# Optimization experiments

Measured on AMD Instinct MI355X. Metric: run time of the kernel, lower is better.

## Reference

```python
import jax, jax.numpy as jnp
import numpy as np

FEAT = 36          # 4 + node_embedding_dim(32)
N_NODES = 24       # max_num_nodes_per_route
N_ROUTES = 48      # max_num_route
CUST_H = 128
CUST_OUT = 32
RNN_H = 128        # route_output_dim
B = 512


def _xavier(key, shape):
    fan_in, fan_out = shape[0], shape[1]
    lim = float(np.sqrt(6.0 / (fan_in + fan_out)))
    return jax.random.uniform(key, shape, jnp.float32, -lim, lim)


def setup_inputs() -> dict:
    key = jax.random.key(0)
    ks = jax.random.split(key, 24)
    inp = {
        "candidates": jax.random.normal(ks[0], (B, 2 * FEAT), jnp.float32),
        "customers": jax.random.normal(ks[1], (B, N_ROUTES, N_NODES * FEAT), jnp.float32),
        # Customer_Model MLP: 36 -> 128 (tanh) -> 32 (tanh)
        "cust_w1": _xavier(ks[2], (FEAT, CUST_H)),
        "cust_b1": jnp.zeros((CUST_H,), jnp.float32),
        "cust_w2": _xavier(ks[3], (CUST_H, CUST_OUT)),
        "cust_b2": jnp.zeros((CUST_OUT,), jnp.float32),
        # GRU layer 0 (input 32 -> hidden 128), gates order (r,z,n)
        "gru_wih0": _xavier(ks[4], (CUST_OUT, 3 * RNN_H)),
        "gru_whh0": _xavier(ks[5], (RNN_H, 3 * RNN_H)),
        "gru_bih0": jnp.zeros((3 * RNN_H,), jnp.float32),
        "gru_bhh0": jnp.zeros((3 * RNN_H,), jnp.float32),
        # GRU layer 1 (128 -> 128)
        "gru_wih1": _xavier(ks[6], (RNN_H, 3 * RNN_H)),
        "gru_whh1": _xavier(ks[7], (RNN_H, 3 * RNN_H)),
        "gru_bih1": jnp.zeros((3 * RNN_H,), jnp.float32),
        "gru_bhh1": jnp.zeros((3 * RNN_H,), jnp.float32),
        # candidate head and final MLP
        "cand_w": _xavier(ks[8], (2 * FEAT, 64)),
        "cand_b": jnp.zeros((64,), jnp.float32),
        "fc1_w": _xavier(ks[9], (RNN_H + 64, 128)),
        "fc1_b": jnp.zeros((128,), jnp.float32),
        "fc2_w": _xavier(ks[10], (128, 128)),
        "fc2_b": jnp.zeros((128,), jnp.float32),
        "fc3_w": _xavier(ks[11], (128, 1)),
        "fc3_b": jnp.zeros((1,), jnp.float32),
    }
    return inp


def _gru_layer(x_seq, wih, whh, bih, bhh):
    # x_seq: [T, N, in_dim]; returns [T, N, RNN_H]
    gi = jnp.einsum('tni,ih->tnh', x_seq, wih) + bih  # precompute input gates

    def step(h, gi_t):
        gh = h @ whh + bhh
        i_r, i_z, i_n = jnp.split(gi_t, 3, axis=-1)
        h_r, h_z, h_n = jnp.split(gh, 3, axis=-1)
        r = jax.nn.sigmoid(i_r + h_r)
        z = jax.nn.sigmoid(i_z + h_z)
        n = jnp.tanh(i_n + r * h_n)
        h_new = (1.0 - z) * n + z * h
        return h_new, h_new

    h0 = jnp.zeros((x_seq.shape[1], RNN_H), x_seq.dtype)
    _, out = jax.lax.scan(step, h0, gi)
    return out


def reference(candidates, customers, cust_w1, cust_b1, cust_w2, cust_b2,
              gru_wih0, gru_whh0, gru_bih0, gru_bhh0,
              gru_wih1, gru_whh1, gru_bih1, gru_bhh1,
              cand_w, cand_b, fc1_w, fc1_b, fc2_w, fc2_b, fc3_w, fc3_b):
    b = candidates.shape[0]
    x_c = candidates @ cand_w + cand_b                      # [B, 64]

    # all routes processed at once: fold routes into batch dim
    x = customers.reshape(b * N_ROUTES, N_NODES, FEAT)
    x = jnp.transpose(x, (1, 0, 2))                          # [T=24, B*48, 36]
    # Customer_Model MLP (tanh hidden, tanh output)
    x = jnp.tanh(jnp.tanh(x @ cust_w1 + cust_b1) @ cust_w2 + cust_b2)  # [24, B*48, 32]

    out = _gru_layer(x, gru_wih0, gru_whh0, gru_bih0, gru_bhh0)
    out = _gru_layer(out, gru_wih1, gru_whh1, gru_bih1, gru_bhh1)
    last = out[-1].reshape(b, N_ROUTES, RNN_H)               # last timestep per route
    x_r = last.mean(axis=1)                                  # mean over 48 routes
    # dropout is identity at inference

    h = jnp.concatenate([x_r, x_c], axis=1)                  # [B, 192]
    h = jnp.tanh(h @ fc1_w + fc1_b)
    h = jnp.tanh(h @ fc2_w + fc2_b)
    return h @ fc3_w + fc3_b                                 # [B, 1]
```

## Files before the change

### kernel.cpp

```cpp
#include <hip/hip_runtime.h>
#include <stdint.h>


#define NSEQ   24576
#define TSTEPS 24
#define SEQB   32

typedef __attribute__((ext_vector_type(8))) short bf16x8;
typedef __attribute__((ext_vector_type(4))) float floatx4;

#define PK_W1    0
#define PK_W2    8192
#define PK_WIH0  12288
#define PK_WHH0  24576
#define PK_WIH1  73728
#define PK_WHH1  122880
#define PK_END   172032
#define X2_EL    172032
#define HOUT_BYTE 38092800

#define MFMA(a,b,c) c = __builtin_amdgcn_mfma_f32_16x16x32_bf16(a, b, c, 0, 0, 0)

__device__ __forceinline__ uint16_t f2bf(float f) {
  uint32_t u = __float_as_uint(f);
  u += 0x7FFFu + ((u >> 16) & 1u);
  return (uint16_t)(u >> 16);
}
__device__ __forceinline__ uint32_t cvt_pk(float a, float b) {
  uint32_t r;
  asm("v_cvt_pk_bf16_f32 %0, %1, %2" : "=v"(r) : "v"(a), "v"(b));
  return r;
}
__device__ __forceinline__ float fast_sigmoid(float x) {
  float e = __builtin_amdgcn_exp2f(-1.4426950408889634f * x);
  return __builtin_amdgcn_rcpf(1.0f + e);
}
__device__ __forceinline__ float fast_tanh(float x) {
  float e = __builtin_amdgcn_exp2f(-2.8853900817779268f * x);
  return 2.0f * __builtin_amdgcn_rcpf(1.0f + e) - 1.0f;
}
__device__ __forceinline__ bf16x8 ldf(const uint16_t* p) {
  return *(const bf16x8*)p;
}

__global__ __launch_bounds__(256) void pack_weights(
    const float* __restrict__ w1, const float* __restrict__ w2,
    const float* __restrict__ wih0, const float* __restrict__ whh0,
    const float* __restrict__ wih1, const float* __restrict__ whh1,
    uint16_t* __restrict__ ws) {
  int idx = blockIdx.x * 256 + threadIdx.x;
  if (idx >= PK_END) return;
  const float* W; int N, KB, Kreal, base;
  if      (idx <  8192) { W = w1;   N = 128; KB = 2; Kreal = 36;  base = 0; }
  else if (idx < 12288) { W = w2;   N = 32;  KB = 4; Kreal = 128; base = 8192; }
  else if (idx < 24576) { W = wih0; N = 384; KB = 1; Kreal = 32;  base = 12288; }
  else if (idx < 73728) { W = whh0; N = 384; KB = 4; Kreal = 128; base = 24576; }
  else if (idx < 122880){ W = wih1; N = 384; KB = 4; Kreal = 128; base = 73728; }
  else                  { W = whh1; N = 384; KB = 4; Kreal = 128; base = 122880; }
  int li = idx - base;
  int frag = li >> 9;
  int e = li & 511;
  int lane = e >> 3, j = e & 7;
  int kb = frag % KB, nt = frag / KB;
  int k = kb * 32 + (lane >> 4) * 8 + j;
  int n = nt * 16 + (lane & 15);
  float v = (k < Kreal) ? W[k * N + n] : 0.0f;
  ws[base + li] = f2bf(v);
}

__global__ __launch_bounds__(256) void mlp_kernel(
    const float* __restrict__ customers, const float* __restrict__ b1,
    const float* __restrict__ b2, const uint16_t* __restrict__ wpk,
    uint16_t* __restrict__ x2out) {
  __shared__ uint16_t sA[128 * 136];
  const int sg = blockIdx.x % 768;
  const int tg = blockIdx.x / 768;
  const int s0 = sg * 32;
  const int t0 = tg * 4;
  const int tid = threadIdx.x;
  const int w = tid >> 6, l = tid & 63, q = l >> 4, c = l & 15;
  const int lo8 = l * 8;
  const int hb = 4 * q;
  const int tw = t0 + w;

  floatx4 acc[2][8];
  #pragma unroll
  for (int mi = 0; mi < 2; ++mi)
    #pragma unroll
    for (int nt = 0; nt < 8; ++nt) acc[mi][nt] = (floatx4){0.f, 0.f, 0.f, 0.f};

  #pragma unroll
  for (int mi = 0; mi < 2; ++mi) {
    const int seq = s0 + mi * 16 + c;
    const float* xp = customers + (size_t)seq * 864 + tw * 36;
    floatx4 u0 = *(const floatx4*)(xp + q * 8);
    floatx4 u1 = *(const floatx4*)(xp + q * 8 + 4);
    bf16x8 a0;
    { uint32_t* a0u = (uint32_t*)&a0;
      a0u[0] = cvt_pk(u0[0], u0[1]); a0u[1] = cvt_pk(u0[2], u0[3]);
      a0u[2] = cvt_pk(u1[0], u1[1]); a0u[3] = cvt_pk(u1[2], u1[3]); }
    bf16x8 a1x = (bf16x8){0,0,0,0,0,0,0,0};
    if (q == 0) {
      floatx4 u2 = *(const floatx4*)(xp + 32);
      uint32_t* a1u = (uint32_t*)&a1x;
      a1u[0] = cvt_pk(u2[0], u2[1]); a1u[1] = cvt_pk(u2[2], u2[3]);
    }
    #pragma unroll
    for (int nt = 0; nt < 8; ++nt) {
      bf16x8 bv0 = ldf(wpk + PK_W1 + (nt * 2 + 0) * 512 + lo8);
      bf16x8 bv1 = ldf(wpk + PK_W1 + (nt * 2 + 1) * 512 + lo8);
      MFMA(bv0, a0,  acc[mi][nt]);
      MFMA(bv1, a1x, acc[mi][nt]);
    }
  }
  #pragma unroll
  for (int mi = 0; mi < 2; ++mi) {
    const int mt = 2 * w + mi;
    #pragma unroll
    for (int nt = 0; nt < 8; ++nt) {
      const floatx4 bv = *(const floatx4*)(b1 + nt * 16 + hb);
      float o0 = fast_tanh(acc[mi][nt][0] + bv[0]);
      float o1 = fast_tanh(acc[mi][nt][1] + bv[1]);
      float o2 = fast_tanh(acc[mi][nt][2] + bv[2]);
      float o3 = fast_tanh(acc[mi][nt][3] + bv[3]);
      uint2 pk; pk.x = cvt_pk(o0, o1); pk.y = cvt_pk(o2, o3);
      *(uint2*)&sA[(mt * 16 + c) * 136 + nt * 16 + hb] = pk;
    }
  }
  __syncthreads();

  floatx4 acc2[2][2];
  #pragma unroll
  for (int mi = 0; mi < 2; ++mi)
    #pragma unroll
    for (int nt = 0; nt < 2; ++nt) acc2[mi][nt] = (floatx4){0.f, 0.f, 0.f, 0.f};

  #pragma unroll
  for (int kb = 0; kb < 4; ++kb) {
    bf16x8 av0 = ldf(&sA[((2 * w + 0) * 16 + c) * 136 + kb * 32 + q * 8]);
    bf16x8 av1 = ldf(&sA[((2 * w + 1) * 16 + c) * 136 + kb * 32 + q * 8]);
    #pragma unroll
    for (int nt = 0; nt < 2; ++nt) {
      bf16x8 bv = ldf(wpk + PK_W2 + (nt * 4 + kb) * 512 + lo8);
      MFMA(bv, av0, acc2[0][nt]);
      MFMA(bv, av1, acc2[1][nt]);
    }
  }
  #pragma unroll
  for (int mi = 0; mi < 2; ++mi) {
    const size_t grow = (size_t)tw * NSEQ + s0 + mi * 16 + c;
    #pragma unroll
    for (int nt = 0; nt < 2; ++nt) {
      const floatx4 bv = *(const floatx4*)(b2 + nt * 16 + hb);
      float o0 = fast_tanh(acc2[mi][nt][0] + bv[0]);
      float o1 = fast_tanh(acc2[mi][nt][1] + bv[1]);
      float o2 = fast_tanh(acc2[mi][nt][2] + bv[2]);
      float o3 = fast_tanh(acc2[mi][nt][3] + bv[3]);
      uint2 pk; pk.x = cvt_pk(o0, o1); pk.y = cvt_pk(o2, o3);
      *(uint2*)(x2out + grow * 32 + nt * 16 + hb) = pk;
    }
  }
}

__global__ __launch_bounds__(512, 2) void gru_res(
    const uint16_t* __restrict__ wpk, const uint16_t* __restrict__ x2,
    const float* __restrict__ bih0, const float* __restrict__ bhh0,
    const float* __restrict__ bih1, const float* __restrict__ bhh1,
    float* __restrict__ hout) {
  __shared__ uint16_t h0l[2][SEQB * 136];
  __shared__ uint16_t h1l[2][SEQB * 136];
  __shared__ float bias_l[8][128];
  const int seq0 = blockIdx.x * SEQB;
  const int tid = threadIdx.x;
  const int J = tid >> 6, l = tid & 63, q = l >> 4, c = l & 15;
  const int lo8 = l * 8;

  for (int i = tid; i < 2176; i += 512) ((uint32_t*)h1l[0])[i] = 0u;
  for (int i = tid; i < 1024; i += 512) {
    int g = i >> 7, k = i & 127;
    float v;
    if      (g == 0) v = bih0[k]       + bhh0[k];
    else if (g == 1) v = bih0[128 + k] + bhh0[128 + k];
    else if (g == 2) v = bih0[256 + k];
    else if (g == 3) v = bhh0[256 + k];
    else if (g == 4) v = bih1[k]       + bhh1[k];
    else if (g == 5) v = bih1[128 + k] + bhh1[128 + k];
    else if (g == 6) v = bih1[256 + k];
    else             v = bhh1[256 + k];
    bias_l[g][k] = v;
  }

  bf16x8 wi0[3], wh0[3][4], wi1[3][4], wh1[3][4];
  #pragma unroll
  for (int g = 0; g < 3; ++g) {
    wi0[g] = ldf(wpk + PK_WIH0 + (g * 8 + J) * 512 + lo8);
    #pragma unroll
    for (int kb = 0; kb < 4; ++kb) {
      wh0[g][kb] = ldf(wpk + PK_WHH0 + ((g * 8 + J) * 4 + kb) * 512 + lo8);
      wi1[g][kb] = ldf(wpk + PK_WIH1 + ((g * 8 + J) * 4 + kb) * 512 + lo8);
      wh1[g][kb] = ldf(wpk + PK_WHH1 + ((g * 8 + J) * 4 + kb) * 512 + lo8);
    }
  }
  const int hb = J * 16 + 4 * q;

  floatx4 h0m0 = (floatx4){0.f,0.f,0.f,0.f}, h0m1 = (floatx4){0.f,0.f,0.f,0.f};
  floatx4 h1m0 = (floatx4){0.f,0.f,0.f,0.f}, h1m1 = (floatx4){0.f,0.f,0.f,0.f};

  bf16x8 ax_0 = ldf(x2 + (size_t)(seq0 + c) * 32 + q * 8);
  bf16x8 ax_1 = ldf(x2 + (size_t)(seq0 + 16 + c) * 32 + q * 8);
  __syncthreads();

  #define GRU_PRO(TI, AX, H0M)                                              \
  {                                                                         \
    floatx4 aR = *(const floatx4*)&bias_l[0][hb];                           \
    floatx4 aZ = *(const floatx4*)&bias_l[1][hb];                           \
    floatx4 aN = *(const floatx4*)&bias_l[2][hb];                           \
    floatx4 aH = *(const floatx4*)&bias_l[3][hb];                           \
    MFMA(wi0[0], AX, aR); MFMA(wi0[1], AX, aZ); MFMA(wi0[2], AX, aN);       \
    float o[4];                                                             \
    _Pragma("unroll")                                                       \
    for (int e = 0; e < 4; ++e) {                                           \
      float r  = fast_sigmoid(aR[e]);                                       \
      float zz = fast_sigmoid(aZ[e]);                                       \
      float nn = fast_tanh(aN[e] + r * aH[e]);                              \
      o[e] = nn - zz * nn;                                                  \
      H0M[e] = o[e];                                                        \
    }                                                                       \
    uint2 pk; pk.x = cvt_pk(o[0], o[1]); pk.y = cvt_pk(o[2], o[3]);         \
    *(uint2*)(h0l[0] + ((TI) * 16 + c) * 136 + hb) = pk;                    \
  }
  GRU_PRO(0, ax_0, h0m0)
  GRU_PRO(1, ax_1, h0m1)
  #undef GRU_PRO
  __syncthreads();

  ax_0 = ldf(x2 + ((size_t)NSEQ + seq0 + c) * 32 + q * 8);
  ax_1 = ldf(x2 + ((size_t)NSEQ + seq0 + 16 + c) * 32 + q * 8);

  #define GRU_TILE(TI, AX, H0M, H1M)                                        \
  {                                                                         \
    floatx4 aR1 = *(const floatx4*)&bias_l[4][hb];                          \
    floatx4 aZ1 = *(const floatx4*)&bias_l[5][hb];                          \
    floatx4 aN1 = *(const floatx4*)&bias_l[6][hb];                          \
    floatx4 aH1 = *(const floatx4*)&bias_l[7][hb];                          \
    floatx4 aR0 = *(const floatx4*)&bias_l[0][hb];                          \
    floatx4 aZ0 = *(const floatx4*)&bias_l[1][hb];                          \
    floatx4 aN0 = *(const floatx4*)&bias_l[2][hb];                          \
    floatx4 aH0 = *(const floatx4*)&bias_l[3][hb];                          \
    _Pragma("unroll")                                                       \
    for (int kb = 0; kb < 4; ++kb) {                                        \
      bf16x8 a0 = ldf(h0cur + ((TI) * 16 + c) * 136 + kb * 32 + q * 8);     \
      bf16x8 ah = ldf(h1prv + ((TI) * 16 + c) * 136 + kb * 32 + q * 8);     \
      MFMA(wi1[0][kb], a0, aR1); MFMA(wh1[0][kb], ah, aR1);                 \
      MFMA(wi1[1][kb], a0, aZ1); MFMA(wh1[1][kb], ah, aZ1);                 \
      MFMA(wi1[2][kb], a0, aN1); MFMA(wh1[2][kb], ah, aH1);                 \
      MFMA(wh0[0][kb], a0, aR0);                                            \
      MFMA(wh0[1][kb], a0, aZ0);                                            \
      MFMA(wh0[2][kb], a0, aH0);                                            \
    }                                                                       \
    MFMA(wi0[0], AX, aR0); MFMA(wi0[1], AX, aZ0); MFMA(wi0[2], AX, aN0);    \
    {                                             \
      float o[4];                                                           \
      _Pragma("unroll")                                                     \
      for (int e = 0; e < 4; ++e) {                                         \
        float r  = fast_sigmoid(aR1[e]);                                    \
        float zz = fast_sigmoid(aZ1[e]);                                    \
        float nn = fast_tanh(aN1[e] + r * aH1[e]);                          \
        o[e] = nn + zz * (H1M[e] - nn);                                     \
        H1M[e] = o[e];                                                      \
      }                                                                     \
      uint2 pk; pk.x = cvt_pk(o[0], o[1]); pk.y = cvt_pk(o[2], o[3]);       \
      *(uint2*)(h1cur + ((TI) * 16 + c) * 136 + hb) = pk;                   \
    }                                                                       \
    {                                           \
      float o[4];                                                           \
      _Pragma("unroll")                                                     \
      for (int e = 0; e < 4; ++e) {                                         \
        float r  = fast_sigmoid(aR0[e]);                                    \
        float zz = fast_sigmoid(aZ0[e]);                                    \
        float nn = fast_tanh(aN0[e] + r * aH0[e]);                          \
        o[e] = nn + zz * (H0M[e] - nn);                                     \
        H0M[e] = o[e];                                                      \
      }                                                                     \
      uint2 pk; pk.x = cvt_pk(o[0], o[1]); pk.y = cvt_pk(o[2], o[3]);       \
      *(uint2*)(h0nxt + ((TI) * 16 + c) * 136 + hb) = pk;                   \
    }                                                                       \
  }

  #pragma unroll 1
  for (int t = 0; t < TSTEPS - 1; ++t) {
    const uint16_t* h0cur = h0l[t & 1];
    const uint16_t* h1prv = h1l[t & 1];
    uint16_t* h0nxt = h0l[(t + 1) & 1];
    uint16_t* h1cur = h1l[(t + 1) & 1];
    const int tnx = (t + 2 < TSTEPS) ? t + 2 : TSTEPS - 1;
    bf16x8 axn_0 = ldf(x2 + ((size_t)tnx * NSEQ + seq0 + c) * 32 + q * 8);
    bf16x8 axn_1 = ldf(x2 + ((size_t)tnx * NSEQ + seq0 + 16 + c) * 32 + q * 8);

    GRU_TILE(0, ax_0, h0m0, h1m0)
    __builtin_amdgcn_sched_barrier(0);
    GRU_TILE(1, ax_1, h0m1, h1m1)

    __syncthreads();
    ax_0 = axn_0; ax_1 = axn_1;
  }
  #undef GRU_TILE

  {
    const int t = TSTEPS - 1;
    const uint16_t* h0cur = h0l[t & 1];
    const uint16_t* h1prv = h1l[t & 1];
    #define GRU_LAST(TI, H1M)                                               \
    {                                                                       \
      floatx4 aR1 = *(const floatx4*)&bias_l[4][hb];                        \
      floatx4 aZ1 = *(const floatx4*)&bias_l[5][hb];                        \
      floatx4 aN1 = *(const floatx4*)&bias_l[6][hb];                        \
      floatx4 aH1 = *(const floatx4*)&bias_l[7][hb];                        \
      _Pragma("unroll")                                                     \
      for (int kb = 0; kb < 4; ++kb) {                                      \
        bf16x8 a0 = ldf(h0cur + ((TI) * 16 + c) * 136 + kb * 32 + q * 8);   \
        bf16x8 ah = ldf(h1prv + ((TI) * 16 + c) * 136 + kb * 32 + q * 8);   \
        MFMA(wi1[0][kb], a0, aR1); MFMA(wh1[0][kb], ah, aR1);               \
        MFMA(wi1[1][kb], a0, aZ1); MFMA(wh1[1][kb], ah, aZ1);               \
        MFMA(wi1[2][kb], a0, aN1); MFMA(wh1[2][kb], ah, aH1);               \
      }                                                                     \
      _Pragma("unroll")                                                     \
      for (int e = 0; e < 4; ++e) {                                         \
        float r  = fast_sigmoid(aR1[e]);                                    \
        float zz = fast_sigmoid(aZ1[e]);                                    \
        float nn = fast_tanh(aN1[e] + r * aH1[e]);                          \
        H1M[e] = nn + zz * (H1M[e] - nn);                                   \
      }                                                                     \
    }
    GRU_LAST(0, h1m0)
    GRU_LAST(1, h1m1)
    #undef GRU_LAST
  }

  *(floatx4*)(hout + (size_t)(seq0 + c) * 128 + hb) = h1m0;
  *(floatx4*)(hout + (size_t)(seq0 + 16 + c) * 128 + hb) = h1m1;
}

__global__ __launch_bounds__(192) void final_kernel(
    const float* __restrict__ hout, const float* __restrict__ cands,
    const float* __restrict__ cw, const float* __restrict__ cb,
    const float* __restrict__ f1w, const float* __restrict__ f1b,
    const float* __restrict__ f2w, const float* __restrict__ f2b,
    const float* __restrict__ f3w, const float* __restrict__ f3b,
    float* __restrict__ out) {
  __shared__ float hc[192];
  __shared__ float v1[128];
  __shared__ float v2[128];
  __shared__ float red[128];
  const int b = blockIdx.x, tid = threadIdx.x;
  if (tid < 128) {
    float s = 0.f;
    const float* hp = hout + (size_t)(b * 48) * 128 + tid;
    #pragma unroll 4
    for (int r = 0; r < 48; ++r) s += hp[r * 128];
    hc[tid] = s * (1.0f / 48.0f);
  } else {
    int j = tid - 128;
    float s = cb[j];
    const float* cp = cands + b * 72;
    #pragma unroll 8
    for (int k = 0; k < 72; ++k) s += cp[k] * cw[k * 64 + j];
    hc[128 + j] = s;
  }
  __syncthreads();
  if (tid < 128) {
    float s = f1b[tid];
    for (int k = 0; k < 192; ++k) s += hc[k] * f1w[k * 128 + tid];
    v1[tid] = fast_tanh(s);
  }
  __syncthreads();
  if (tid < 128) {
    float s = f2b[tid];
    for (int k = 0; k < 128; ++k) s += v1[k] * f2w[k * 128 + tid];
    v2[tid] = fast_tanh(s);
  }
  __syncthreads();
  if (tid < 128) red[tid] = v2[tid] * f3w[tid];
  __syncthreads();
  if (tid < 64) {
    float s = red[tid] + red[tid + 64];
    s += __shfl_down(s, 32);
    s += __shfl_down(s, 16);
    s += __shfl_down(s, 8);
    s += __shfl_down(s, 4);
    s += __shfl_down(s, 2);
    s += __shfl_down(s, 1);
    if (tid == 0) out[b] = s + f3b[0];
  }
}

extern "C" void kernel_launch(void* const* d_in, const int* in_sizes, int n_in,
                              void* d_out, int out_size, void* d_ws, size_t ws_size,
                              hipStream_t stream) {
  const float* cand  = (const float*)d_in[0];
  const float* cust  = (const float*)d_in[1];
  const float* w1    = (const float*)d_in[2];
  const float* b1    = (const float*)d_in[3];
  const float* w2    = (const float*)d_in[4];
  const float* b2    = (const float*)d_in[5];
  const float* wih0  = (const float*)d_in[6];
  const float* whh0  = (const float*)d_in[7];
  const float* bih0  = (const float*)d_in[8];
  const float* bhh0  = (const float*)d_in[9];
  const float* wih1  = (const float*)d_in[10];
  const float* whh1  = (const float*)d_in[11];
  const float* bih1  = (const float*)d_in[12];
  const float* bhh1  = (const float*)d_in[13];
  const float* cw    = (const float*)d_in[14];
  const float* cb    = (const float*)d_in[15];
  const float* f1w   = (const float*)d_in[16];
  const float* f1b   = (const float*)d_in[17];
  const float* f2w   = (const float*)d_in[18];
  const float* f2b   = (const float*)d_in[19];
  const float* f3w   = (const float*)d_in[20];
  const float* f3b   = (const float*)d_in[21];

  uint16_t* wsp = (uint16_t*)d_ws;
  uint16_t* x2p = wsp + X2_EL;
  float* hout = (float*)((char*)d_ws + HOUT_BYTE);
  float* outp = (float*)d_out;

  pack_weights<<<(PK_END + 255) / 256, 256, 0, stream>>>(w1, w2, wih0, whh0, wih1, whh1, wsp);
  mlp_kernel<<<(NSEQ * TSTEPS) / 128, 256, 0, stream>>>(cust, b1, b2, wsp, x2p);
  gru_res<<<NSEQ / SEQB, 512, 0, stream>>>(wsp, x2p, bih0, bhh0, bih1, bhh1, hout);
  final_kernel<<<512, 192, 0, stream>>>(hout, cand, cw, cb, f1w, f1b, f2w, f2b, f3w, f3b, outp);
}
```

Baseline: 407.2 us.

## Fuse customer MLP into GRU kernel, keeping MLP outputs in LDS

Merges the separate customer-MLP kernel into the GRU kernel. Each block first computes the 36→128→32 tanh MLP for its 32 sequences across all 24 timesteps, with each of 8 waves handling 3 timesteps, and stores the bf16 results in a shared LDS region. The GRU recurrence then reads its per-step inputs from LDS rather than global memory. This removes one kernel launch plus the global write and reread of the intermediate activations. In exchange LDS use grows to about 116 KB per block, which can cap occupancy, and the MLP phase runs serially before the recurrence inside each block.

```diff
diff --git a/kernel.cpp b/kernel.cpp
--- a/kernel.cpp
+++ b/kernel.cpp
@@ -16,8 +16,13 @@
 #define PK_WIH1  73728
 #define PK_WHH1  122880
 #define PK_END   172032
-#define X2_EL    172032
 #define HOUT_BYTE 38092800
+
+#define SCR_EL   4352
+#define H1L_EL   8704
+#define BIAS_EL  17408
+#define X2L_EL   34816
+#define LDS_EL   59392
 
 #define MFMA(a,b,c) c = __builtin_amdgcn_mfma_f32_16x16x32_bf16(a, b, c, 0, 0, 0)
 
@@ -68,114 +73,104 @@
   ws[base + li] = f2bf(v);
 }
 
-__global__ __launch_bounds__(256) void mlp_kernel(
+__global__ __launch_bounds__(512, 2) void gru_fused(
     const float* __restrict__ customers, const float* __restrict__ b1,
     const float* __restrict__ b2, const uint16_t* __restrict__ wpk,
-    uint16_t* __restrict__ x2out) {
-  __shared__ uint16_t sA[128 * 136];
-  const int sg = blockIdx.x % 768;
-  const int tg = blockIdx.x / 768;
-  const int s0 = sg * 32;
-  const int t0 = tg * 4;
-  const int tid = threadIdx.x;
-  const int w = tid >> 6, l = tid & 63, q = l >> 4, c = l & 15;
-  const int lo8 = l * 8;
-  const int hb = 4 * q;
-  const int tw = t0 + w;
-
-  floatx4 acc[2][8];
-  #pragma unroll
-  for (int mi = 0; mi < 2; ++mi)
-    #pragma unroll
-    for (int nt = 0; nt < 8; ++nt) acc[mi][nt] = (floatx4){0.f, 0.f, 0.f, 0.f};
-
-  #pragma unroll
-  for (int mi = 0; mi < 2; ++mi) {
-    const int seq = s0 + mi * 16 + c;
-    const float* xp = customers + (size_t)seq * 864 + tw * 36;
-    floatx4 u0 = *(const floatx4*)(xp + q * 8);
-    floatx4 u1 = *(const floatx4*)(xp + q * 8 + 4);
-    bf16x8 a0;
-    { uint32_t* a0u = (uint32_t*)&a0;
-      a0u[0] = cvt_pk(u0[0], u0[1]); a0u[1] = cvt_pk(u0[2], u0[3]);
-      a0u[2] = cvt_pk(u1[0], u1[1]); a0u[3] = cvt_pk(u1[2], u1[3]); }
-    bf16x8 a1x = (bf16x8){0,0,0,0,0,0,0,0};
-    if (q == 0) {
-      floatx4 u2 = *(const floatx4*)(xp + 32);
-      uint32_t* a1u = (uint32_t*)&a1x;
-      a1u[0] = cvt_pk(u2[0], u2[1]); a1u[1] = cvt_pk(u2[2], u2[3]);
-    }
-    #pragma unroll
-    for (int nt = 0; nt < 8; ++nt) {
-      bf16x8 bv0 = ldf(wpk + PK_W1 + (nt * 2 + 0) * 512 + lo8);
-      bf16x8 bv1 = ldf(wpk + PK_W1 + (nt * 2 + 1) * 512 + lo8);
-      MFMA(bv0, a0,  acc[mi][nt]);
-      MFMA(bv1, a1x, acc[mi][nt]);
-    }
-  }
-  #pragma unroll
-  for (int mi = 0; mi < 2; ++mi) {
-    const int mt = 2 * w + mi;
-    #pragma unroll
-    for (int nt = 0; nt < 8; ++nt) {
-      const floatx4 bv = *(const floatx4*)(b1 + nt * 16 + hb);
-      float o0 = fast_tanh(acc[mi][nt][0] + bv[0]);
-      float o1 = fast_tanh(acc[mi][nt][1] + bv[1]);
-      float o2 = fast_tanh(acc[mi][nt][2] + bv[2]);
-      float o3 = fast_tanh(acc[mi][nt][3] + bv[3]);
-      uint2 pk; pk.x = cvt_pk(o0, o1); pk.y = cvt_pk(o2, o3);
-      *(uint2*)&sA[(mt * 16 + c) * 136 + nt * 16 + hb] = pk;
-    }
-  }
-  __syncthreads();
-
-  floatx4 acc2[2][2];
-  #pragma unroll
-  for (int mi = 0; mi < 2; ++mi)
-    #pragma unroll
-    for (int nt = 0; nt < 2; ++nt) acc2[mi][nt] = (floatx4){0.f, 0.f, 0.f, 0.f};
-
-  #pragma unroll
-  for (int kb = 0; kb < 4; ++kb) {
-    bf16x8 av0 = ldf(&sA[((2 * w + 0) * 16 + c) * 136 + kb * 32 + q * 8]);
-    bf16x8 av1 = ldf(&sA[((2 * w + 1) * 16 + c) * 136 + kb * 32 + q * 8]);
-    #pragma unroll
-    for (int nt = 0; nt < 2; ++nt) {
-      bf16x8 bv = ldf(wpk + PK_W2 + (nt * 4 + kb) * 512 + lo8);
-      MFMA(bv, av0, acc2[0][nt]);
-      MFMA(bv, av1, acc2[1][nt]);
-    }
-  }
-  #pragma unroll
-  for (int mi = 0; mi < 2; ++mi) {
-    const size_t grow = (size_t)tw * NSEQ + s0 + mi * 16 + c;
-    #pragma unroll
-    for (int nt = 0; nt < 2; ++nt) {
-      const floatx4 bv = *(const floatx4*)(b2 + nt * 16 + hb);
-      float o0 = fast_tanh(acc2[mi][nt][0] + bv[0]);
-      float o1 = fast_tanh(acc2[mi][nt][1] + bv[1]);
-      float o2 = fast_tanh(acc2[mi][nt][2] + bv[2]);
-      float o3 = fast_tanh(acc2[mi][nt][3] + bv[3]);
-      uint2 pk; pk.x = cvt_pk(o0, o1); pk.y = cvt_pk(o2, o3);
-      *(uint2*)(x2out + grow * 32 + nt * 16 + hb) = pk;
-    }
-  }
-}
-
-__global__ __launch_bounds__(512, 2) void gru_res(
-    const uint16_t* __restrict__ wpk, const uint16_t* __restrict__ x2,
     const float* __restrict__ bih0, const float* __restrict__ bhh0,
     const float* __restrict__ bih1, const float* __restrict__ bhh1,
     float* __restrict__ hout) {
-  __shared__ uint16_t h0l[2][SEQB * 136];
-  __shared__ uint16_t h1l[2][SEQB * 136];
-  __shared__ float bias_l[8][128];
+  __shared__ __align__(16) uint16_t lds[LDS_EL];
   const int seq0 = blockIdx.x * SEQB;
   const int tid = threadIdx.x;
   const int J = tid >> 6, l = tid & 63, q = l >> 4, c = l & 15;
   const int lo8 = l * 8;
-
-  for (int i = tid; i < 2176; i += 512) ((uint32_t*)h1l[0])[i] = 0u;
+  const int hbA = 4 * q;
+  const int hb  = J * 16 + 4 * q;
+
+  {
+    uint16_t* scr = lds + J * SCR_EL;
+    uint16_t* x2l = lds + X2L_EL;
+    #pragma unroll 1
+    for (int tt = 0; tt < 3; ++tt) {
+      const int t = J * 3 + tt;
+      floatx4 acc[2][8];
+      #pragma unroll
+      for (int mi = 0; mi < 2; ++mi)
+        #pragma unroll
+        for (int nt = 0; nt < 8; ++nt) acc[mi][nt] = (floatx4){0.f, 0.f, 0.f, 0.f};
+
+      #pragma unroll
+      for (int mi = 0; mi < 2; ++mi) {
+        const int seq = seq0 + mi * 16 + c;
+        const float* xp = customers + (size_t)seq * 864 + t * 36;
+        floatx4 u0 = *(const floatx4*)(xp + q * 8);
+        floatx4 u1 = *(const floatx4*)(xp + q * 8 + 4);
+        bf16x8 a0;
+        { uint32_t* a0u = (uint32_t*)&a0;
+          a0u[0] = cvt_pk(u0[0], u0[1]); a0u[1] = cvt_pk(u0[2], u0[3]);
+          a0u[2] = cvt_pk(u1[0], u1[1]); a0u[3] = cvt_pk(u1[2], u1[3]); }
+        bf16x8 a1x = (bf16x8){0,0,0,0,0,0,0,0};
+        if (q == 0) {
+          floatx4 u2 = *(const floatx4*)(xp + 32);
+          uint32_t* a1u = (uint32_t*)&a1x;
+          a1u[0] = cvt_pk(u2[0], u2[1]); a1u[1] = cvt_pk(u2[2], u2[3]);
+        }
+        #pragma unroll
+        for (int nt = 0; nt < 8; ++nt) {
+          bf16x8 bv0 = ldf(wpk + PK_W1 + (nt * 2 + 0) * 512 + lo8);
+          bf16x8 bv1 = ldf(wpk + PK_W1 + (nt * 2 + 1) * 512 + lo8);
+          MFMA(bv0, a0,  acc[mi][nt]);
+          MFMA(bv1, a1x, acc[mi][nt]);
+        }
+      }
+      #pragma unroll
+      for (int mi = 0; mi < 2; ++mi)
+        #pragma unroll
+        for (int nt = 0; nt < 8; ++nt) {
+          const floatx4 bv = *(const floatx4*)(b1 + nt * 16 + hbA);
+          float o0 = fast_tanh(acc[mi][nt][0] + bv[0]);
+          float o1 = fast_tanh(acc[mi][nt][1] + bv[1]);
+          float o2 = fast_tanh(acc[mi][nt][2] + bv[2]);
+          float o3 = fast_tanh(acc[mi][nt][3] + bv[3]);
+          uint2 pk; pk.x = cvt_pk(o0, o1); pk.y = cvt_pk(o2, o3);
+          *(uint2*)&scr[(mi * 16 + c) * 136 + nt * 16 + hbA] = pk;
+        }
+      floatx4 acc2[2][2];
+      #pragma unroll
+      for (int mi = 0; mi < 2; ++mi)
+        #pragma unroll
+        for (int nt = 0; nt < 2; ++nt) acc2[mi][nt] = (floatx4){0.f, 0.f, 0.f, 0.f};
+      #pragma unroll
+      for (int kb = 0; kb < 4; ++kb) {
+        bf16x8 av0 = ldf(&scr[(c)      * 136 + kb * 32 + q * 8]);
+        bf16x8 av1 = ldf(&scr[(16 + c) * 136 + kb * 32 + q * 8]);
+        #pragma unroll
+        for (int nt = 0; nt < 2; ++nt) {
+          bf16x8 bv = ldf(wpk + PK_W2 + (nt * 4 + kb) * 512 + lo8);
+          MFMA(bv, av0, acc2[0][nt]);
+          MFMA(bv, av1, acc2[1][nt]);
+        }
+      }
+      #pragma unroll
+      for (int mi = 0; mi < 2; ++mi)
+        #pragma unroll
+        for (int nt = 0; nt < 2; ++nt) {
+          const floatx4 bv = *(const floatx4*)(b2 + nt * 16 + hbA);
+          float o0 = fast_tanh(acc2[mi][nt][0] + bv[0]);
+          float o1 = fast_tanh(acc2[mi][nt][1] + bv[1]);
+          float o2 = fast_tanh(acc2[mi][nt][2] + bv[2]);
+          float o3 = fast_tanh(acc2[mi][nt][3] + bv[3]);
+          uint2 pk; pk.x = cvt_pk(o0, o1); pk.y = cvt_pk(o2, o3);
+          *(uint2*)&x2l[t * 1024 + (mi * 16 + c) * 32 + nt * 16 + hbA] = pk;
+        }
+    }
+  }
+  __syncthreads();
+  __builtin_amdgcn_sched_barrier(0);
+
+  const uint16_t* x2l = lds + X2L_EL;
+  for (int i = tid; i < 2176; i += 512) ((uint32_t*)(lds + H1L_EL))[i] = 0u;
+  float* biasf = (float*)(lds + BIAS_EL);
   for (int i = tid; i < 1024; i += 512) {
     int g = i >> 7, k = i & 127;
     float v;
@@ -187,7 +182,7 @@
     else if (g == 5) v = bih1[128 + k] + bhh1[128 + k];
     else if (g == 6) v = bih1[256 + k];
     else             v = bhh1[256 + k];
-    bias_l[g][k] = v;
+    biasf[g * 128 + k] = v;
   }
 
   bf16x8 wi0[3], wh0[3][4], wi1[3][4], wh1[3][4];
@@ -201,52 +196,50 @@
       wh1[g][kb] = ldf(wpk + PK_WHH1 + ((g * 8 + J) * 4 + kb) * 512 + lo8);
     }
   }
-  const int hb = J * 16 + 4 * q;
 
   floatx4 h0m0 = (floatx4){0.f,0.f,0.f,0.f}, h0m1 = (floatx4){0.f,0.f,0.f,0.f};
   floatx4 h1m0 = (floatx4){0.f,0.f,0.f,0.f}, h1m1 = (floatx4){0.f,0.f,0.f,0.f};
 
-  bf16x8 ax_0 = ldf(x2 + (size_t)(seq0 + c) * 32 + q * 8);
-  bf16x8 ax_1 = ldf(x2 + (size_t)(seq0 + 16 + c) * 32 + q * 8);
-  __syncthreads();
-
-  #define GRU_PRO(TI, AX, H0M)                                              \
-  {                                                                         \
-    floatx4 aR = *(const floatx4*)&bias_l[0][hb];                           \
-    floatx4 aZ = *(const floatx4*)&bias_l[1][hb];                           \
-    floatx4 aN = *(const floatx4*)&bias_l[2][hb];                           \
-    floatx4 aH = *(const floatx4*)&bias_l[3][hb];                           \
-    MFMA(wi0[0], AX, aR); MFMA(wi0[1], AX, aZ); MFMA(wi0[2], AX, aN);       \
-    float o[4];                                                             \
-    _Pragma("unroll")                                                       \
-    for (int e = 0; e < 4; ++e) {                                           \
-      float r  = fast_sigmoid(aR[e]);                                       \
-      float zz = fast_sigmoid(aZ[e]);                                       \
-      float nn = fast_tanh(aN[e] + r * aH[e]);                              \
-      o[e] = nn - zz * nn;                                                  \
-      H0M[e] = o[e];                                                        \
-    }                                                                       \
-    uint2 pk; pk.x = cvt_pk(o[0], o[1]); pk.y = cvt_pk(o[2], o[3]);         \
-    *(uint2*)(h0l[0] + ((TI) * 16 + c) * 136 + hb) = pk;                    \
-  }
-  GRU_PRO(0, ax_0, h0m0)
-  GRU_PRO(1, ax_1, h0m1)
-  #undef GRU_PRO
-  __syncthreads();
-
-  ax_0 = ldf(x2 + ((size_t)NSEQ + seq0 + c) * 32 + q * 8);
-  ax_1 = ldf(x2 + ((size_t)NSEQ + seq0 + 16 + c) * 32 + q * 8);
+  __syncthreads();
+
+  {
+    bf16x8 ax_0 = ldf(x2l + (c)      * 32 + q * 8);
+    bf16x8 ax_1 = ldf(x2l + (16 + c) * 32 + q * 8);
+    #define GRU_PRO(TI, AX, H0M)                                            \
+    {                                                                       \
+      floatx4 aR = *(const floatx4*)&biasf[0 * 128 + hb];                   \
+      floatx4 aZ = *(const floatx4*)&biasf[1 * 128 + hb];                   \
+      floatx4 aN = *(const floatx4*)&biasf[2 * 128 + hb];                   \
+      floatx4 aH = *(const floatx4*)&biasf[3 * 128 + hb];                   \
+      MFMA(wi0[0], AX, aR); MFMA(wi0[1], AX, aZ); MFMA(wi0[2], AX, aN);     \
+      float o[4];                                                           \
+      _Pragma("unroll")                                                     \
+      for (int e = 0; e < 4; ++e) {                                         \
+        float r  = fast_sigmoid(aR[e]);                                     \
+        float zz = fast_sigmoid(aZ[e]);                                     \
+        float nn = fast_tanh(aN[e] + r * aH[e]);                            \
+        o[e] = nn - zz * nn;                                                \
+        H0M[e] = o[e];                                                      \
+      }                                                                     \
+      uint2 pk; pk.x = cvt_pk(o[0], o[1]); pk.y = cvt_pk(o[2], o[3]);       \
+      *(uint2*)(lds + ((TI) * 16 + c) * 136 + hb) = pk;                     \
+    }
+    GRU_PRO(0, ax_0, h0m0)
+    GRU_PRO(1, ax_1, h0m1)
+    #undef GRU_PRO
+  }
+  __syncthreads();
 
   #define GRU_TILE(TI, AX, H0M, H1M)                                        \
   {                                                                         \
-    floatx4 aR1 = *(const floatx4*)&bias_l[4][hb];                          \
-    floatx4 aZ1 = *(const floatx4*)&bias_l[5][hb];                          \
-    floatx4 aN1 = *(const floatx4*)&bias_l[6][hb];                          \
-    floatx4 aH1 = *(const floatx4*)&bias_l[7][hb];                          \
-    floatx4 aR0 = *(const floatx4*)&bias_l[0][hb];                          \
-    floatx4 aZ0 = *(const floatx4*)&bias_l[1][hb];                          \
-    floatx4 aN0 = *(const floatx4*)&bias_l[2][hb];                          \
-    floatx4 aH0 = *(const floatx4*)&bias_l[3][hb];                          \
+    floatx4 aR1 = *(const floatx4*)&biasf[4 * 128 + hb];                    \
+    floatx4 aZ1 = *(const floatx4*)&biasf[5 * 128 + hb];                    \
+    floatx4 aN1 = *(const floatx4*)&biasf[6 * 128 + hb];                    \
+    floatx4 aH1 = *(const floatx4*)&biasf[7 * 128 + hb];                    \
+    floatx4 aR0 = *(const floatx4*)&biasf[0 * 128 + hb];                    \
+    floatx4 aZ0 = *(const floatx4*)&biasf[1 * 128 + hb];                    \
+    floatx4 aN0 = *(const floatx4*)&biasf[2 * 128 + hb];                    \
+    floatx4 aH0 = *(const floatx4*)&biasf[3 * 128 + hb];                    \
     _Pragma("unroll")                                                       \
     for (int kb = 0; kb < 4; ++kb) {                                        \
       bf16x8 a0 = ldf(h0cur + ((TI) * 16 + c) * 136 + kb * 32 + q * 8);     \
@@ -289,33 +282,30 @@
 
   #pragma unroll 1
   for (int t = 0; t < TSTEPS - 1; ++t) {
-    const uint16_t* h0cur = h0l[t & 1];
-    const uint16_t* h1prv = h1l[t & 1];
-    uint16_t* h0nxt = h0l[(t + 1) & 1];
-    uint16_t* h1cur = h1l[(t + 1) & 1];
-    const int tnx = (t + 2 < TSTEPS) ? t + 2 : TSTEPS - 1;
-    bf16x8 axn_0 = ldf(x2 + ((size_t)tnx * NSEQ + seq0 + c) * 32 + q * 8);
-    bf16x8 axn_1 = ldf(x2 + ((size_t)tnx * NSEQ + seq0 + 16 + c) * 32 + q * 8);
+    uint16_t* h0cur = lds + (t & 1) * SCR_EL;
+    uint16_t* h1prv = lds + H1L_EL + (t & 1) * SCR_EL;
+    uint16_t* h0nxt = lds + ((t + 1) & 1) * SCR_EL;
+    uint16_t* h1cur = lds + H1L_EL + ((t + 1) & 1) * SCR_EL;
+    bf16x8 ax_0 = ldf(x2l + (t + 1) * 1024 + (c)      * 32 + q * 8);
+    bf16x8 ax_1 = ldf(x2l + (t + 1) * 1024 + (16 + c) * 32 + q * 8);
 
     GRU_TILE(0, ax_0, h0m0, h1m0)
     __builtin_amdgcn_sched_barrier(0);
     GRU_TILE(1, ax_1, h0m1, h1m1)
 
     __syncthreads();
-    ax_0 = axn_0; ax_1 = axn_1;
   }
   #undef GRU_TILE
 
   {
-    const int t = TSTEPS - 1;
-    const uint16_t* h0cur = h0l[t & 1];
-    const uint16_t* h1prv = h1l[t & 1];
+    const uint16_t* h0cur = lds + ((TSTEPS - 1) & 1) * SCR_EL;
+    const uint16_t* h1prv = lds + H1L_EL + ((TSTEPS - 1) & 1) * SCR_EL;
     #define GRU_LAST(TI, H1M)                                               \
     {                                                                       \
-      floatx4 aR1 = *(const floatx4*)&bias_l[4][hb];                        \
-      floatx4 aZ1 = *(const floatx4*)&bias_l[5][hb];                        \
-      floatx4 aN1 = *(const floatx4*)&bias_l[6][hb];                        \
-      floatx4 aH1 = *(const floatx4*)&bias_l[7][hb];                        \
+      floatx4 aR1 = *(const floatx4*)&biasf[4 * 128 + hb];                  \
+      floatx4 aZ1 = *(const floatx4*)&biasf[5 * 128 + hb];                  \
+      floatx4 aN1 = *(const floatx4*)&biasf[6 * 128 + hb];                  \
+      floatx4 aH1 = *(const floatx4*)&biasf[7 * 128 + hb];                  \
       _Pragma("unroll")                                                     \
       for (int kb = 0; kb < 4; ++kb) {                                      \
         bf16x8 a0 = ldf(h0cur + ((TI) * 16 + c) * 136 + kb * 32 + q * 8);   \
@@ -421,12 +411,10 @@
   const float* f3b   = (const float*)d_in[21];
 
   uint16_t* wsp = (uint16_t*)d_ws;
-  uint16_t* x2p = wsp + X2_EL;
   float* hout = (float*)((char*)d_ws + HOUT_BYTE);
   float* outp = (float*)d_out;
 
   pack_weights<<<(PK_END + 255) / 256, 256, 0, stream>>>(w1, w2, wih0, whh0, wih1, whh1, wsp);
-  mlp_kernel<<<(NSEQ * TSTEPS) / 128, 256, 0, stream>>>(cust, b1, b2, wsp, x2p);
-  gru_res<<<NSEQ / SEQB, 512, 0, stream>>>(wsp, x2p, bih0, bhh0, bih1, bhh1, hout);
+  gru_fused<<<NSEQ / SEQB, 512, 0, stream>>>(cust, b1, b2, wsp, bih0, bhh0, bih1, bhh1, hout);
   final_kernel<<<512, 192, 0, stream>>>(hout, cand, cw, cb, f1w, f1b, f2w, f2b, f3w, f3b, outp);
 }
```

Result: no change. 404.4 us (-0.7%).
